# Optimization experiments

Measured on AMD Instinct MI355X. Metric: run time of the kernel, lower is better.

Reference implementation:

```python
import jax, jax.numpy as jnp
import numpy as np

N = 100000
E = 800000
NFEAT = 128
NHID = 128
NCLASS = 40
THRESHOLD = 0.1
EPS = 1e-8


def setup_inputs() -> dict:
    key = jax.random.key(0)
    ks = jax.random.split(key, 12)
    x = jax.random.normal(ks[0], (N, NFEAT), dtype=jnp.float32)
    edge_index = jax.random.randint(ks[1], (2, E), 0, N, dtype=jnp.int64)
    edge_index2 = jax.random.randint(ks[2], (2, E), 0, N, dtype=jnp.int64)
    s1 = 1.0 / np.sqrt(NFEAT)
    s2 = 1.0 / np.sqrt(NHID)
    s3 = 1.0 / np.sqrt(NCLASS)
    W_gc1 = jax.random.uniform(ks[3], (NFEAT, NHID), jnp.float32, -s1, s1)
    b_gc1 = jax.random.uniform(ks[4], (NHID,), jnp.float32, -s1, s1)
    W_gc2 = jax.random.uniform(ks[5], (NHID, NCLASS), jnp.float32, -s2, s2)
    b_gc2 = jax.random.uniform(ks[6], (NCLASS,), jnp.float32, -s2, s2)
    W_att1 = jax.random.uniform(ks[7], (NCLASS, NCLASS), jnp.float32, -s3, s3)
    b_att1 = jax.random.uniform(ks[8], (NCLASS,), jnp.float32, -s3, s3)
    W_att2 = jax.random.uniform(ks[9], (NCLASS, 1), jnp.float32, -s3, s3)
    return {"x": x, "W_gc1": W_gc1, "b_gc1": b_gc1, "W_gc2": W_gc2,
            "b_gc2": b_gc2, "W_att1": W_att1, "b_att1": b_att1,
            "W_att2": W_att2, "edge_index": edge_index, "edge_index2": edge_index2}


def att_coef(feat, row, col, alive):
    # cosine similarity per edge; edges failing the threshold get weight 0
    # (exactly equivalent to removing them: contribute 0 to degree & messages).
    a = feat[row]          # [E, d]
    b = feat[col]          # [E, d]
    dot = jnp.sum(a * b, axis=-1)
    na = jnp.maximum(jnp.linalg.norm(a, axis=-1), EPS)
    nb = jnp.maximum(jnp.linalg.norm(b, axis=-1), EPS)
    sims = dot / (na * nb)
    mask = alive & (sims >= THRESHOLD)
    # original computes this under torch.no_grad()
    ew = jax.lax.stop_gradient(jnp.where(mask, sims, 0.0))
    return ew, mask


def gcn_conv(x, row, col, ew, W, b):
    # PyG GCNConv with add_self_loops=True, normalize=True on weighted adjacency
    h = x @ W                                     # [N, out]
    deg = jax.ops.segment_sum(ew, row, num_segments=N) + 1.0  # +1 self loop
    dinv = deg ** -0.5
    nw = dinv[row] * ew * dinv[col]               # [E]
    agg = jax.ops.segment_sum(h[col] * nw[:, None], row, num_segments=N)
    agg = agg + h * (dinv * dinv)[:, None]        # self-loop contribution
    return agg + b


def reference(x, W_gc1, b_gc1, W_gc2, b_gc2, W_att1, b_att1, W_att2,
              edge_index, edge_index2):
    r1, c1 = edge_index[0], edge_index[1]
    r2, c2 = edge_index2[0], edge_index2[1]
    ones = jnp.ones((E,), dtype=bool)

    ew2, m2 = att_coef(x, r2, c2, ones)
    ew1, m1 = att_coef(x, r1, c1, ones)

    x2 = jax.nn.relu(gcn_conv(x, r2, c2, ew2, W_gc1, b_gc1))
    x1 = jax.nn.relu(gcn_conv(x, r1, c1, ew1, W_gc1, b_gc1))
    # dropout is identity at eval time

    ew2b, _ = att_coef(x2, r2, c2, m2)
    ew1b, _ = att_coef(x1, r1, c1, m1)

    x2 = gcn_conv(x2, r2, c2, ew2b, W_gc2, b_gc2)
    x1 = gcn_conv(x1, r1, c1, ew1b, W_gc2, b_gc2)

    z = jnp.stack([x1, x2], axis=1)               # [N, 2, C]
    w = jnp.tanh(z @ W_att1 + b_att1) @ W_att2    # [N, 2, 1]
    beta = jax.nn.softmax(w, axis=1)
    fused = jnp.sum(beta * z, axis=1)             # [N, C]
    return jax.nn.log_softmax(fused, axis=1)
```

## Files before the change

### kernel.cpp

```cpp
#include <hip/hip_runtime.h>
#include <hip/hip_bf16.h>

#define NN 100000
#define EE 800000
#define THRV 0.1f
#define DELTA 0.008f
#define EPSV 1e-8f

#define ATOMIC_ADD_F32 unsafeAtomicAdd

__device__ inline int dot4(int a, int b, int c) {
#if __has_builtin(__builtin_amdgcn_sdot4)
    return __builtin_amdgcn_sdot4(a, b, c, false);
#else
    int s = c;
    #pragma unroll
    for (int k = 0; k < 4; k++) {
        int av = (a << (24 - 8 * k)) >> 24;
        int bv = (b << (24 - 8 * k)) >> 24;
        s += av * bv;
    }
    return s;
#endif
}

__device__ inline unsigned short f2bf(float f) {
    unsigned int u = __float_as_uint(f);
    u += 0x7fffu + ((u >> 16) & 1u);
    return (unsigned short)(u >> 16);
}

__device__ inline float bf2f(unsigned short s) {
    return __uint_as_float(((unsigned int)s) << 16);
}


__global__ __launch_bounds__(256) void normalize_k(const float* __restrict__ x,
                                                   unsigned short* __restrict__ xq,
                                                   float* __restrict__ rs,
                                                   float* __restrict__ norms_x,
                                                   float* __restrict__ degL1,
                                                   int* __restrict__ cnt) {
    int node = blockIdx.x * 4 + (threadIdx.x >> 6);
    int lane = threadIdx.x & 63;
    float2 v = reinterpret_cast<const float2*>(x)[(size_t)node * 64 + lane];
    float ss = v.x * v.x + v.y * v.y;
    float am = fmaxf(fabsf(v.x), fabsf(v.y));
    #pragma unroll
    for (int off = 32; off; off >>= 1) {
        ss += __shfl_xor(ss, off);
        am = fmaxf(am, __shfl_xor(am, off));
    }
    float norm = fmaxf(sqrtf(ss), EPSV);
    am = fmaxf(am, 1e-12f);
    float qs = 127.0f / am;
    int q0 = __float2int_rn(v.x * qs);
    int q1 = __float2int_rn(v.y * qs);
    xq[(size_t)node * 64 + lane] = (unsigned short)((q0 & 0xff) | ((q1 & 0xff) << 8));
    if (lane == 0) {
        norms_x[node] = norm;
        rs[node] = am / (127.0f * norm);
        degL1[node] = 1.0f;
        degL1[node + NN] = 1.0f;
        cnt[node] = 0;
        cnt[node + NN] = 0;
    }
}


__global__ __launch_bounds__(128) void quantW_k(const float* __restrict__ W,
                                                int* __restrict__ Wq,
                                                float* __restrict__ wcs) {
    int col = threadIdx.x;
    float am = 0.f;
    for (int k = 0; k < 128; k++) am = fmaxf(am, fabsf(W[k * 128 + col]));
    am = fmaxf(am, 1e-20f);
    float qs = 127.0f / am;
    for (int k4 = 0; k4 < 32; k4++) {
        int p = 0;
        #pragma unroll
        for (int t = 0; t < 4; t++) {
            int q = __float2int_rn(W[(4 * k4 + t) * 128 + col] * qs);
            p |= (q & 0xff) << (8 * t);
        }
        Wq[k4 * 128 + col] = p;
    }
    wcs[col] = am / 127.0f;
}


__global__ __launch_bounds__(256) void edge_sim1_k(
        const unsigned short* __restrict__ xq, const float* __restrict__ rs,
        const float* __restrict__ x, const float* __restrict__ norms_x,
        const int* __restrict__ r1, const int* __restrict__ c1,
        const int* __restrict__ r2, const int* __restrict__ c2,
        float* __restrict__ ews, float* __restrict__ degL1,
        int* __restrict__ cnt) {
    int tid = threadIdx.x;
    int e = blockIdx.x * 32 + (tid >> 3);
    int q = tid & 7;
    int rnode, cnode, gr;
    if (e < EE) { rnode = r1[e]; cnode = c1[e]; gr = rnode; }
    else { int ee = e - EE; rnode = r2[ee]; cnode = c2[ee]; gr = NN + rnode; }
    int role = q >> 2;
    int j = q & 3;
    int node = role ? cnode : rnode;
    const uint4* base = reinterpret_cast<const uint4*>(xq) + (size_t)node * 8 + j * 2;
    uint4 v0 = base[0];
    uint4 v1 = base[1];
    uint4 p0, p1;
    p0.x = (unsigned)__shfl_xor((int)v0.x, 4);
    p0.y = (unsigned)__shfl_xor((int)v0.y, 4);
    p0.z = (unsigned)__shfl_xor((int)v0.z, 4);
    p0.w = (unsigned)__shfl_xor((int)v0.w, 4);
    p1.x = (unsigned)__shfl_xor((int)v1.x, 4);
    p1.y = (unsigned)__shfl_xor((int)v1.y, 4);
    p1.z = (unsigned)__shfl_xor((int)v1.z, 4);
    p1.w = (unsigned)__shfl_xor((int)v1.w, 4);
    int d = dot4((int)v0.x, (int)p0.x, 0);
    d = dot4((int)v0.y, (int)p0.y, d);
    d = dot4((int)v0.z, (int)p0.z, d);
    d = dot4((int)v0.w, (int)p0.w, d);
    d = dot4((int)v1.x, (int)p1.x, d);
    d = dot4((int)v1.y, (int)p1.y, d);
    d = dot4((int)v1.z, (int)p1.z, d);
    d = dot4((int)v1.w, (int)p1.w, d);
    d += __shfl_xor(d, 1);
    d += __shfl_xor(d, 2);
    float sim = (float)d * rs[rnode] * rs[cnode];
    if (fabsf(sim - THRV) <= DELTA) {
        const float4* xa = reinterpret_cast<const float4*>(x + (size_t)rnode * 128);
        const float4* xb = reinterpret_cast<const float4*>(x + (size_t)cnode * 128);
        float df = 0.f;
        #pragma unroll
        for (int t = 0; t < 4; t++) {
            float4 a = xa[q + 8 * t];
            float4 bb = xb[q + 8 * t];
            df += a.x * bb.x + a.y * bb.y + a.z * bb.z + a.w * bb.w;
        }
        df += __shfl_xor(df, 1);
        df += __shfl_xor(df, 2);
        df += __shfl_xor(df, 4);
        sim = df / (norms_x[rnode] * norms_x[cnode]);
    }
    float w = (sim >= THRV) ? sim : 0.0f;
    if (q == 0) {
        ews[e] = w;
        if (w != 0.0f) {
            ATOMIC_ADD_F32(&degL1[gr], w);
            atomicAdd(&cnt[gr], 1);
        }
    }
}


__global__ __launch_bounds__(256) void gemm_nh_k(const int* __restrict__ xqi,
                                                 const float* __restrict__ rs,
                                                 const float* __restrict__ norms_x,
                                                 const int* __restrict__ Wq,
                                                 const float* __restrict__ wcs,
                                                 unsigned int* __restrict__ hq,
                                                 float* __restrict__ hrs, int n) {
    __shared__ int WsQ[32 * 128];
    __shared__ int XsQ[32 * 32];
    __shared__ float wcss[128];
    int tid = threadIdx.x;
    int row0 = blockIdx.x * 32;
    {
        int4* W4 = reinterpret_cast<int4*>(WsQ);
        const int4* Wg4 = reinterpret_cast<const int4*>(Wq);
        #pragma unroll
        for (int i = 0; i < 4; i++) W4[tid + 256 * i] = Wg4[tid + 256 * i];
        if (tid < 128) wcss[tid] = wcs[tid];
        int r = tid >> 3, p = tid & 7;
        reinterpret_cast<int4*>(XsQ)[tid] =
            reinterpret_cast<const int4*>(xqi + (size_t)(row0 + r) * 32)[p];
    }
    __syncthreads();
    int cg = tid & 31;
    int rl = tid >> 5;
    int4 acc[4];
    #pragma unroll
    for (int i = 0; i < 4; i++) acc[i] = make_int4(0, 0, 0, 0);
    for (int k4 = 0; k4 < 32; k4++) {
        int4 wv = reinterpret_cast<const int4*>(WsQ + k4 * 128)[cg];
        #pragma unroll
        for (int r4 = 0; r4 < 4; r4++) {
            int xv = XsQ[(rl + 8 * r4) * 32 + k4];
            acc[r4].x = dot4(xv, wv.x, acc[r4].x);
            acc[r4].y = dot4(xv, wv.y, acc[r4].y);
            acc[r4].z = dot4(xv, wv.z, acc[r4].z);
            acc[r4].w = dot4(xv, wv.w, acc[r4].w);
        }
    }
    float4 wc = reinterpret_cast<const float4*>(wcss)[cg];
    #pragma unroll
    for (int r4 = 0; r4 < 4; r4++) {
        int grow = row0 + rl + 8 * r4;
        float xscale = rs[grow] * norms_x[grow];
        float fx = (float)acc[r4].x * xscale * wc.x;
        float fy = (float)acc[r4].y * xscale * wc.y;
        float fz = (float)acc[r4].z * xscale * wc.z;
        float fw = (float)acc[r4].w * xscale * wc.w;
        float am = fmaxf(fmaxf(fabsf(fx), fabsf(fy)), fmaxf(fabsf(fz), fabsf(fw)));
        #pragma unroll
        for (int off = 1; off < 32; off <<= 1) am = fmaxf(am, __shfl_xor(am, off));
        am = fmaxf(am, 1e-20f);
        float qs = 127.0f / am;
        int q0 = __float2int_rn(fx * qs);
        int q1 = __float2int_rn(fy * qs);
        int q2 = __float2int_rn(fz * qs);
        int q3 = __float2int_rn(fw * qs);
        unsigned int u = (q0 & 0xff) | ((q1 & 0xff) << 8) |
                         ((q2 & 0xff) << 16) | ((q3 & 0xff) << 24);
        if (grow < n) {
            hq[(size_t)grow * 32 + cg] = u;
            if (cg == 0) hrs[grow] = am / 127.0f;
        }
    }
}


__global__ __launch_bounds__(512) void scan1_k(const int* __restrict__ in,
                                               int* __restrict__ out,
                                               int* __restrict__ partials, int n) {
    __shared__ int a[1024], b[1024];
    int t = threadIdx.x;
    int base = blockIdx.x * 1024;
    a[t]       = (base + t       < n) ? in[base + t]       : 0;
    a[t + 512] = (base + t + 512 < n) ? in[base + t + 512] : 0;
    __syncthreads();
    int* src = a; int* dst = b;
    for (int off = 1; off < 1024; off <<= 1) {
        #pragma unroll
        for (int q = 0; q < 2; q++) {
            int i = t + q * 512;
            int v = src[i];
            if (i >= off) v += src[i - off];
            dst[i] = v;
        }
        __syncthreads();
        int* tmp = src; src = dst; dst = tmp;
    }
    for (int q = 0; q < 2; q++) {
        int i = t + q * 512;
        if (base + i < n) out[base + i] = i ? src[i - 1] : 0;
    }
    if (t == 0) partials[blockIdx.x] = src[1023];
}

__global__ __launch_bounds__(256) void scan2_k(int* __restrict__ partials, int m) {
    __shared__ int a[256], b[256];
    int t = threadIdx.x;
    a[t] = (t < m) ? partials[t] : 0;
    __syncthreads();
    int* src = a; int* dst = b;
    for (int off = 1; off < 256; off <<= 1) {
        int v = src[t];
        if (t >= off) v += src[t - off];
        dst[t] = v;
        __syncthreads();
        int* tmp = src; src = dst; dst = tmp;
    }
    if (t < m) partials[t] = t ? src[t - 1] : 0;
}

__global__ void scan3_k(int* __restrict__ start, int* __restrict__ next,
                        const int* __restrict__ partials,
                        const int* __restrict__ cnt, int n) {
    int i = blockIdx.x * 256 + threadIdx.x;
    if (i < n) {
        int v = start[i] + partials[i >> 10];
        start[i] = v;
        next[i] = v;
        if (i == n - 1) start[n] = v + cnt[i];
    }
}


__global__ void scatter_alive_k(const int* __restrict__ r1, const int* __restrict__ c1,
                                const int* __restrict__ r2, const int* __restrict__ c2,
                                const float* __restrict__ ews,
                                const float* __restrict__ degL1,
                                const float* __restrict__ hrs,
                                int* __restrict__ next, int2* __restrict__ acw) {
    int e = blockIdx.x * 256 + threadIdx.x;
    float w = ews[e];
    if (w == 0.0f) return;
    int gr, c, sb;
    if (e < EE) { gr = r1[e]; c = c1[e]; sb = 0; }
    else        { gr = NN + r2[e - EE]; c = c2[e - EE]; sb = NN; }
    int pos = atomicAdd(&next[gr], 1);
    int2 rec;
    rec.x = c;
    rec.y = __float_as_int(w * rsqrtf(degL1[sb + c]) * hrs[c]);
    acw[pos] = rec;
}


__global__ __launch_bounds__(256) void agg128_fused_k(
        const unsigned short* __restrict__ hq16, const float* __restrict__ hrs,
        const int* __restrict__ start, const int2* __restrict__ acw,
        const float* __restrict__ degL1, const float* __restrict__ bias,
        unsigned int* __restrict__ aggb, unsigned short* __restrict__ xq2,
        float* __restrict__ rs2, float* __restrict__ norms_l2,
        float* __restrict__ degL2) {
    int gr = blockIdx.x * 4 + (threadIdx.x >> 6);
    int lane = threadIdx.x & 63;
    int rnode = (gr < NN) ? gr : gr - NN;
    int j0 = start[gr], j1 = start[gr + 1];
    float2 acc = make_float2(0.f, 0.f);
    for (int j = j0; j < j1; j++) {
        int2 rec = acw[j];
        float wv = __int_as_float(rec.y);
        unsigned short hv = hq16[(size_t)rec.x * 64 + lane];
        acc.x += (float)(char)(hv & 0xff) * wv;
        acc.y += (float)(char)(hv >> 8) * wv;
    }
    float dr = rsqrtf(degL1[gr]);
    float hr = hrs[rnode];
    unsigned short hs = hq16[(size_t)rnode * 64 + lane];
    float hx = (float)(char)(hs & 0xff) * hr;
    float hy = (float)(char)(hs >> 8) * hr;
    float2 bb = reinterpret_cast<const float2*>(bias)[lane];
    float vx = fmaxf(acc.x * dr + hx * dr * dr + bb.x, 0.0f);
    float vy = fmaxf(acc.y * dr + hy * dr * dr + bb.y, 0.0f);
    aggb[(size_t)gr * 64 + lane] =
        (unsigned int)f2bf(vx) | ((unsigned int)f2bf(vy) << 16);
    float ss = vx * vx + vy * vy;
    float am = fmaxf(vx, vy);
    #pragma unroll
    for (int off = 32; off; off >>= 1) {
        ss += __shfl_xor(ss, off);
        am = fmaxf(am, __shfl_xor(am, off));
    }
    float norm = fmaxf(sqrtf(ss), EPSV);
    am = fmaxf(am, 1e-12f);
    float qs = 127.0f / am;
    int q0 = __float2int_rn(vx * qs);
    int q1 = __float2int_rn(vy * qs);
    xq2[(size_t)gr * 64 + lane] = (unsigned short)((q0 & 0xff) | ((q1 & 0xff) << 8));
    if (lane == 0) {
        rs2[gr] = am / (127.0f * norm);
        norms_l2[gr] = norm;
        degL2[gr] = 1.0f;
    }
}


__global__ __launch_bounds__(256) void edge_sim2_k(
        const unsigned short* __restrict__ xq2, const float* __restrict__ rs2,
        const unsigned int* __restrict__ aggb, const float* __restrict__ norms_l2,
        const int* __restrict__ start, int2* __restrict__ acw,
        float* __restrict__ degL2) {
    int gr = blockIdx.x * 4 + (threadIdx.x >> 6);
    int lane = threadIdx.x & 63;
    int j0 = start[gr], j1 = start[gr + 1];
    if (j0 == j1) return;
    int set_base = (gr < NN) ? 0 : NN;
    unsigned int au = xq2[(size_t)gr * 64 + lane];
    int a0 = ((int)(au << 24)) >> 24;
    int a1 = ((int)((au << 16) & 0xff000000u)) >> 24;
    float ra = rs2[gr];
    float nr = norms_l2[gr];
    float sum = 0.f;
    for (int j = j0; j < j1; j++) {
        int2 rec = acw[j];
        int cg = set_base + rec.x;
        unsigned int bu = xq2[(size_t)cg * 64 + lane];
        int b0 = ((int)(bu << 24)) >> 24;
        int b1 = ((int)((bu << 16) & 0xff000000u)) >> 24;
        int d = a0 * b0 + a1 * b1;
        #pragma unroll
        for (int off = 32; off; off >>= 1) d += __shfl_xor(d, off);
        float sim = (float)d * ra * rs2[cg];
        if (fabsf(sim - THRV) <= DELTA) {
            unsigned int av = aggb[(size_t)gr * 64 + lane];
            unsigned int bv = aggb[(size_t)cg * 64 + lane];
            float df = bf2f((unsigned short)(av & 0xffff)) *
                       bf2f((unsigned short)(bv & 0xffff)) +
                       bf2f((unsigned short)(av >> 16)) *
                       bf2f((unsigned short)(bv >> 16));
            #pragma unroll
            for (int off = 32; off; off >>= 1) df += __shfl_xor(df, off);
            sim = df / (nr * norms_l2[cg]);
        }
        float w2 = (sim >= THRV) ? sim : 0.0f;
        if (lane == 0) acw[j].y = __float_as_int(w2);
        sum += w2;
    }
    if (lane == 0) degL2[gr] = 1.0f + sum;
}


__global__ __launch_bounds__(256) void gemm_nc_k(const unsigned short* __restrict__ Ab,
                                                 const float* __restrict__ W,
                                                 unsigned short* __restrict__ Cb, int n) {
    __shared__ float Ws[128 * 40];
    __shared__ float Xs[64 * 130];
    int tid = threadIdx.x;
    int row0 = blockIdx.x * 64;
    for (int i = tid; i < 128 * 40; i += 256) Ws[i] = W[i];
    #pragma unroll
    for (int i = 0; i < 4; i++) {
        int idx = tid + 256 * i;
        int rr = idx >> 4, kq = idx & 15;
        int grow = row0 + rr; if (grow >= n) grow = n - 1;
        uint4 v = reinterpret_cast<const uint4*>(Ab + (size_t)grow * 128)[kq];
        float* dst = &Xs[rr * 130 + kq * 8];
        dst[0] = bf2f((unsigned short)(v.x & 0xffff));
        dst[1] = bf2f((unsigned short)(v.x >> 16));
        dst[2] = bf2f((unsigned short)(v.y & 0xffff));
        dst[3] = bf2f((unsigned short)(v.y >> 16));
        dst[4] = bf2f((unsigned short)(v.z & 0xffff));
        dst[5] = bf2f((unsigned short)(v.z >> 16));
        dst[6] = bf2f((unsigned short)(v.w & 0xffff));
        dst[7] = bf2f((unsigned short)(v.w >> 16));
    }
    __syncthreads();
    int c5 = tid & 7;
    int r  = tid >> 3;
    float acc0[5] = {0, 0, 0, 0, 0}, acc1[5] = {0, 0, 0, 0, 0};
    for (int k = 0; k < 128; k++) {
        float x0 = Xs[r * 130 + k], x1 = Xs[(r + 32) * 130 + k];
        #pragma unroll
        for (int c = 0; c < 5; c++) {
            float wv = Ws[k * 40 + c5 * 5 + c];
            acc0[c] += x0 * wv; acc1[c] += x1 * wv;
        }
    }
    int g0 = row0 + r, g1 = row0 + r + 32;
    if (g0 < n) {
        for (int c = 0; c < 5; c++)
            Cb[(size_t)g0 * 64 + c5 * 5 + c] = f2bf(acc0[c]);
    }
    if (g1 < n) {
        for (int c = 0; c < 5; c++)
            Cb[(size_t)g1 * 64 + c5 * 5 + c] = f2bf(acc1[c]);
    }
}


__global__ __launch_bounds__(256) void agg40_fused_k(
        const unsigned short* __restrict__ h2b, const int* __restrict__ start,
        const int2* __restrict__ acw, const float* __restrict__ degL2,
        const float* __restrict__ bias, float* __restrict__ aggy) {
    int gr = blockIdx.x * 4 + (threadIdx.x >> 6);
    int lane = threadIdx.x & 63;
    int set_base = (gr < NN) ? 0 : NN;
    int j0 = start[gr], j1 = start[gr + 1];
    bool act = lane < 40;
    float acc = 0.f;
    for (int j = j0; j < j1; j++) {
        int2 rec = acw[j];
        float w2 = __int_as_float(rec.y);
        if (w2 == 0.0f) continue;
        int cg = set_base + rec.x;
        float nv = w2 * rsqrtf(degL2[cg]);
        float hv = act ? bf2f(h2b[(size_t)cg * 64 + lane]) : 0.f;
        acc += hv * nv;
    }
    if (act) {
        float dr = rsqrtf(degL2[gr]);
        float self = bf2f(h2b[(size_t)gr * 64 + lane]);
        aggy[(size_t)gr * 40 + lane] = acc * dr + self * dr * dr + bias[lane];
    }
}


__global__ __launch_bounds__(256) void fusion_k(const float* __restrict__ y1,
                                                const float* __restrict__ y2,
                                                const float* __restrict__ W1,
                                                const float* __restrict__ b1,
                                                const float* __restrict__ W2,
                                                float* __restrict__ out, int n) {
    __shared__ float W1s[40 * 40];
    __shared__ float b1s[40];
    __shared__ float W2s[40];
    int tid = threadIdx.x;
    for (int i = tid; i < 1600; i += 256) W1s[i] = W1[i];
    if (tid < 40) { b1s[tid] = b1[tid]; W2s[tid] = W2[tid]; }
    __syncthreads();
    int i = blockIdx.x * 256 + tid;
    if (i >= n) return;
    float z1[40], z2[40];
    const float4* y14 = reinterpret_cast<const float4*>(y1 + (size_t)i * 40);
    const float4* y24 = reinterpret_cast<const float4*>(y2 + (size_t)i * 40);
    #pragma unroll
    for (int q = 0; q < 10; q++) {
        float4 a = y14[q], b = y24[q];
        z1[4 * q] = a.x; z1[4 * q + 1] = a.y; z1[4 * q + 2] = a.z; z1[4 * q + 3] = a.w;
        z2[4 * q] = b.x; z2[4 * q + 1] = b.y; z2[4 * q + 2] = b.z; z2[4 * q + 3] = b.w;
    }
    float w1 = 0.f, w2 = 0.f;
    for (int c = 0; c < 40; c++) {
        float s1 = b1s[c], s2 = b1s[c];
        for (int j = 0; j < 40; j++) {
            float ww = W1s[j * 40 + c];
            s1 += z1[j] * ww; s2 += z2[j] * ww;
        }
        float wa = W2s[c];
        w1 += tanhf(s1) * wa; w2 += tanhf(s2) * wa;
    }
    float m = fmaxf(w1, w2);
    float e1 = expf(w1 - m), e2 = expf(w2 - m);
    float inv = 1.0f / (e1 + e2);
    float be1 = e1 * inv, be2 = e2 * inv;
    float fu[40];
    float mx = -1e30f;
    #pragma unroll
    for (int c = 0; c < 40; c++) {
        fu[c] = be1 * z1[c] + be2 * z2[c];
        mx = fmaxf(mx, fu[c]);
    }
    float se = 0.f;
    #pragma unroll
    for (int c = 0; c < 40; c++) se += expf(fu[c] - mx);
    float ls = logf(se);
    float4* o4 = reinterpret_cast<float4*>(out + (size_t)i * 40);
    #pragma unroll
    for (int q = 0; q < 10; q++) {
        float4 v;
        v.x = fu[4 * q] - mx - ls; v.y = fu[4 * q + 1] - mx - ls;
        v.z = fu[4 * q + 2] - mx - ls; v.w = fu[4 * q + 3] - mx - ls;
        o4[q] = v;
    }
}


extern "C" void kernel_launch(void* const* d_in, const int* in_sizes, int n_in,
                              void* d_out, int out_size, void* d_ws, size_t ws_size,
                              hipStream_t stream) {
    (void)in_sizes; (void)n_in; (void)out_size; (void)ws_size;
    const float* x   = (const float*)d_in[0];
    const float* Wg1 = (const float*)d_in[1];
    const float* bg1 = (const float*)d_in[2];
    const float* Wg2 = (const float*)d_in[3];
    const float* bg2 = (const float*)d_in[4];
    const float* Wa1 = (const float*)d_in[5];
    const float* ba1 = (const float*)d_in[6];
    const float* Wa2 = (const float*)d_in[7];
    const int* ei1 = (const int*)d_in[8];
    const int* ei2 = (const int*)d_in[9];
    const int *r1 = ei1, *c1 = ei1 + EE;
    const int *r2 = ei2, *c2 = ei2 + EE;
    float* out = (float*)d_out;

    float* wp = (float*)d_ws;
    float* norms_x  = wp;  wp += NN;
    float* norms_l2 = wp;  wp += 2 * NN;
    float* rs       = wp;  wp += NN;
    float* degL1    = wp;  wp += 2 * NN;
    float* degL2    = wp;  wp += 2 * NN;
    float* hrs      = wp;  wp += NN;
    int*   cnt      = (int*)wp;  wp += 2 * NN;
    int*   start    = (int*)wp;  wp += 2 * NN + 8;
    int*   next     = (int*)wp;  wp += 2 * NN;
    int*   partials = (int*)wp;  wp += 512;
    int*   Wq       = (int*)wp;  wp += 32 * 128;
    float* wcs      = wp;  wp += 128;
    float* ews      = wp;  wp += 2 * EE;
    int2*  acw      = (int2*)wp; wp += (size_t)2 * 2 * EE;
    unsigned int* hq = (unsigned int*)wp; wp += (size_t)NN * 32;
    unsigned short* h2b = (unsigned short*)wp; wp += (size_t)2 * NN * 32;
    unsigned int*   aggb = (unsigned int*)wp;  wp += (size_t)2 * NN * 64;
    unsigned short* xq2 = (unsigned short*)wp; wp += (size_t)2 * NN * 32;
    unsigned short* xq = (unsigned short*)aggb;
    float* rs2 = ews;
    float* aggy = (float*)aggb;

    const int twoN = 2 * NN;
    const int twoE = 2 * EE;
    const int scan_blocks = (twoN + 1023) / 1024;

    quantW_k<<<1, 128, 0, stream>>>(Wg1, Wq, wcs);
    normalize_k<<<NN / 4, 256, 0, stream>>>(x, xq, rs, norms_x, degL1, cnt);
    edge_sim1_k<<<twoE / 32, 256, 0, stream>>>(xq, rs, x, norms_x,
                                               r1, c1, r2, c2, ews, degL1, cnt);
    gemm_nh_k<<<(NN + 31) / 32, 256, 0, stream>>>((const int*)xq, rs, norms_x,
                                                  Wq, wcs, hq, hrs, NN);

    scan1_k<<<scan_blocks, 512, 0, stream>>>(cnt, start, partials, twoN);
    scan2_k<<<1, 256, 0, stream>>>(partials, scan_blocks);
    scan3_k<<<(twoN + 255) / 256, 256, 0, stream>>>(start, next, partials, cnt, twoN);
    scatter_alive_k<<<twoE / 256, 256, 0, stream>>>(r1, c1, r2, c2, ews, degL1, hrs,
                                                    next, acw);

    agg128_fused_k<<<twoN / 4, 256, 0, stream>>>((const unsigned short*)hq, hrs,
                                                 start, acw, degL1, bg1,
                                                 aggb, xq2, rs2, norms_l2, degL2);

    edge_sim2_k<<<twoN / 4, 256, 0, stream>>>(xq2, rs2, aggb, norms_l2,
                                              start, acw, degL2);
    gemm_nc_k<<<twoN / 64, 256, 0, stream>>>((const unsigned short*)aggb, Wg2,
                                             h2b, twoN);
    agg40_fused_k<<<twoN / 4, 256, 0, stream>>>(h2b, start, acw, degL2, bg2, aggy);
    fusion_k<<<(NN + 255) / 256, 256, 0, stream>>>(aggy, aggy + (size_t)NN * 40,
                                                   Wa1, ba1, Wa2, out, NN);
}
```

Before: 465.4 us.

## Compute second-layer GEMM with int8 dot4 on quantized hidden features

The second GCN layer's dense product now reads the int8-quantized layer-1 output (xq2) and an int8-quantized W_gc2, using sdot4 integer accumulation and rescaling by per-row and per-column scales. It replaces the bf16-load plus fp32 FMA path and halves the bytes loaded per row. The W quantization kernel is generalized to any column count and parallelized across blocks. The cost is extra quantization error in the layer-2 features, and the row-bound guards were dropped.

```diff
diff --git a/kernel.cpp b/kernel.cpp
--- a/kernel.cpp
+++ b/kernel.cpp
@@ -68,24 +68,26 @@
 }
 
 
-__global__ __launch_bounds__(128) void quantW_k(const float* __restrict__ W,
-                                                int* __restrict__ Wq,
-                                                float* __restrict__ wcs) {
-    int col = threadIdx.x;
-    float am = 0.f;
-    for (int k = 0; k < 128; k++) am = fmaxf(am, fabsf(W[k * 128 + col]));
+__global__ __launch_bounds__(64) void quantW_k(const float* __restrict__ W, int C,
+                                               int* __restrict__ Wq,
+                                               float* __restrict__ wcs) {
+    int col = blockIdx.x;
+    int t = threadIdx.x;
+    float am = fmaxf(fabsf(W[t * C + col]), fabsf(W[(t + 64) * C + col]));
+    #pragma unroll
+    for (int off = 32; off; off >>= 1) am = fmaxf(am, __shfl_xor(am, off));
     am = fmaxf(am, 1e-20f);
     float qs = 127.0f / am;
-    for (int k4 = 0; k4 < 32; k4++) {
+    if (t < 32) {
         int p = 0;
         #pragma unroll
-        for (int t = 0; t < 4; t++) {
-            int q = __float2int_rn(W[(4 * k4 + t) * 128 + col] * qs);
-            p |= (q & 0xff) << (8 * t);
-        }
-        Wq[k4 * 128 + col] = p;
-    }
-    wcs[col] = am / 127.0f;
+        for (int tt = 0; tt < 4; tt++) {
+            int q = __float2int_rn(W[(4 * t + tt) * C + col] * qs);
+            p |= (q & 0xff) << (8 * tt);
+        }
+        Wq[t * C + col] = p;
+    }
+    if (t == 0) wcs[col] = am / 127.0f;
 }
 
 
@@ -393,50 +395,52 @@
 }
 
 
-__global__ __launch_bounds__(256) void gemm_nc_k(const unsigned short* __restrict__ Ab,
-                                                 const float* __restrict__ W,
-                                                 unsigned short* __restrict__ Cb, int n) {
-    __shared__ float Ws[128 * 40];
-    __shared__ float Xs[64 * 130];
+__global__ __launch_bounds__(256) void gemm_nc_k(const int* __restrict__ xq2i,
+                                                 const float* __restrict__ rs2,
+                                                 const float* __restrict__ norms_l2,
+                                                 const int* __restrict__ Wq2,
+                                                 const float* __restrict__ wcs2,
+                                                 unsigned short* __restrict__ h2b, int n) {
+    __shared__ int XsQ[64 * 33];
+    __shared__ int WsQ2[32 * 40];
+    __shared__ float wcss[40];
+    __shared__ float rsc[64];
     int tid = threadIdx.x;
     int row0 = blockIdx.x * 64;
-    for (int i = tid; i < 128 * 40; i += 256) Ws[i] = W[i];
-    #pragma unroll
-    for (int i = 0; i < 4; i++) {
+    for (int i = tid; i < 32 * 40; i += 256) WsQ2[i] = Wq2[i];
+    if (tid < 40) wcss[tid] = wcs2[tid];
+    if (tid < 64) {
+        int g = row0 + tid;
+        rsc[tid] = rs2[g] * norms_l2[g];
+    }
+    #pragma unroll
+    for (int i = 0; i < 2; i++) {
         int idx = tid + 256 * i;
-        int rr = idx >> 4, kq = idx & 15;
-        int grow = row0 + rr; if (grow >= n) grow = n - 1;
-        uint4 v = reinterpret_cast<const uint4*>(Ab + (size_t)grow * 128)[kq];
-        float* dst = &Xs[rr * 130 + kq * 8];
-        dst[0] = bf2f((unsigned short)(v.x & 0xffff));
-        dst[1] = bf2f((unsigned short)(v.x >> 16));
-        dst[2] = bf2f((unsigned short)(v.y & 0xffff));
-        dst[3] = bf2f((unsigned short)(v.y >> 16));
-        dst[4] = bf2f((unsigned short)(v.z & 0xffff));
-        dst[5] = bf2f((unsigned short)(v.z >> 16));
-        dst[6] = bf2f((unsigned short)(v.w & 0xffff));
-        dst[7] = bf2f((unsigned short)(v.w >> 16));
+        int rr = idx >> 3, p = idx & 7;
+        int4 v = reinterpret_cast<const int4*>(xq2i + (size_t)(row0 + rr) * 32)[p];
+        int* dst = &XsQ[rr * 33 + p * 4];
+        dst[0] = v.x; dst[1] = v.y; dst[2] = v.z; dst[3] = v.w;
     }
     __syncthreads();
     int c5 = tid & 7;
     int r  = tid >> 3;
-    float acc0[5] = {0, 0, 0, 0, 0}, acc1[5] = {0, 0, 0, 0, 0};
-    for (int k = 0; k < 128; k++) {
-        float x0 = Xs[r * 130 + k], x1 = Xs[(r + 32) * 130 + k];
+    int acc0[5] = {0, 0, 0, 0, 0}, acc1[5] = {0, 0, 0, 0, 0};
+    for (int k4 = 0; k4 < 32; k4++) {
+        int xv0 = XsQ[r * 33 + k4];
+        int xv1 = XsQ[(r + 32) * 33 + k4];
         #pragma unroll
         for (int c = 0; c < 5; c++) {
-            float wv = Ws[k * 40 + c5 * 5 + c];
-            acc0[c] += x0 * wv; acc1[c] += x1 * wv;
-        }
-    }
+            int wv = WsQ2[k4 * 40 + c5 * 5 + c];
+            acc0[c] = dot4(xv0, wv, acc0[c]);
+            acc1[c] = dot4(xv1, wv, acc1[c]);
+        }
+    }
+    float s0 = rsc[r], s1 = rsc[r + 32];
     int g0 = row0 + r, g1 = row0 + r + 32;
-    if (g0 < n) {
-        for (int c = 0; c < 5; c++)
-            Cb[(size_t)g0 * 64 + c5 * 5 + c] = f2bf(acc0[c]);
-    }
-    if (g1 < n) {
-        for (int c = 0; c < 5; c++)
-            Cb[(size_t)g1 * 64 + c5 * 5 + c] = f2bf(acc1[c]);
+    for (int c = 0; c < 5; c++) {
+        float wc = wcss[c5 * 5 + c];
+        h2b[(size_t)g0 * 64 + c5 * 5 + c] = f2bf((float)acc0[c] * s0 * wc);
+        h2b[(size_t)g1 * 64 + c5 * 5 + c] = f2bf((float)acc1[c] * s1 * wc);
     }
 }
 
@@ -559,6 +563,8 @@
     int*   partials = (int*)wp;  wp += 512;
     int*   Wq       = (int*)wp;  wp += 32 * 128;
     float* wcs      = wp;  wp += 128;
+    int*   Wq2      = (int*)wp;  wp += 32 * 40;
+    float* wcs2     = wp;  wp += 40;
     float* ews      = wp;  wp += 2 * EE;
     int2*  acw      = (int2*)wp; wp += (size_t)2 * 2 * EE;
     unsigned int* hq = (unsigned int*)wp; wp += (size_t)NN * 32;
@@ -573,7 +579,8 @@
     const int twoE = 2 * EE;
     const int scan_blocks = (twoN + 1023) / 1024;
 
-    quantW_k<<<1, 128, 0, stream>>>(Wg1, Wq, wcs);
+    quantW_k<<<128, 64, 0, stream>>>(Wg1, 128, Wq, wcs);
+    quantW_k<<<40, 64, 0, stream>>>(Wg2, 40, Wq2, wcs2);
     normalize_k<<<NN / 4, 256, 0, stream>>>(x, xq, rs, norms_x, degL1, cnt);
     edge_sim1_k<<<twoE / 32, 256, 0, stream>>>(xq, rs, x, norms_x,
                                                r1, c1, r2, c2, ews, degL1, cnt);
@@ -592,8 +599,8 @@
 
     edge_sim2_k<<<twoN / 4, 256, 0, stream>>>(xq2, rs2, aggb, norms_l2,
                                               start, acw, degL2);
-    gemm_nc_k<<<twoN / 64, 256, 0, stream>>>((const unsigned short*)aggb, Wg2,
-                                             h2b, twoN);
+    gemm_nc_k<<<twoN / 64, 256, 0, stream>>>((const int*)xq2, rs2, norms_l2,
+                                             Wq2, wcs2, h2b, twoN);
     agg40_fused_k<<<twoN / 4, 256, 0, stream>>>(h2b, start, acw, degL2, bg2, aggy);
     fusion_k<<<(NN + 255) / 256, 256, 0, stream>>>(aggy, aggy + (size_t)NN * 40,
                                                    Wa1, ba1, Wa2, out, NN);
```

Result: faster. 417.0 us (-10.4%).
